# Kernel tuning notes

Hardware: AMD Instinct MI355X
Metric: run time of the kernel (lower is better)

The kernel has to match this reference:

```python
import jax, jax.numpy as jnp
import numpy as np
from jax import lax


def _gather_xq(x_flat, qx, qy, w):
    # x_flat: [B, C, H*W]; qx, qy: [B, H, W] int32 -> [B, C, H, W]
    b, c, _ = x_flat.shape
    h, ww = qx.shape[1], qx.shape[2]
    idx = (qx * w + qy).reshape(b, 1, h * ww)  # [B,1,H*W]
    out = jnp.take_along_axis(x_flat, jnp.broadcast_to(idx, (b, c, h * ww)), axis=2)
    return out.reshape(b, c, h, ww)


def setup_inputs() -> dict:
    key = jax.random.key(0)
    k1, k2 = jax.random.split(key)
    B, C, H, W = 8, 256, 128, 128
    x = jax.random.normal(k1, (B, C, H, W), dtype=jnp.float32)
    w_conv = jax.random.normal(k2, (2, C, 3, 3), dtype=jnp.float32) * 0.02
    b_conv = jnp.zeros((2,), dtype=jnp.float32)
    return {"x": x, "w_conv": w_conv, "b_conv": b_conv}


def reference(x, w_conv, b_conv):
    B, C, H, W = x.shape
    # offset conv: Conv2d(inc, 2, k=3, stride=1, padding=1)
    offset = lax.conv_general_dilated(
        x, w_conv, window_strides=(1, 1), padding=((1, 1), (1, 1)),
        dimension_numbers=("NCHW", "OIHW", "NCHW"),
    ) + b_conv[None, :, None, None]  # [B, 2, H, W], N = 1

    # base grid p_0 (ij indexing as in torch.meshgrid legacy)
    p0_x = jnp.arange(H, dtype=x.dtype)[:, None] * jnp.ones((1, W), dtype=x.dtype)
    p0_y = jnp.ones((H, 1), dtype=x.dtype) * jnp.arange(W, dtype=x.dtype)[None, :]
    px = p0_x[None] + offset[:, 0]  # [B, H, W]
    py = p0_y[None] + offset[:, 1]

    px = jnp.clip(px, 0.0, H - 2)
    py = jnp.clip(py, 0.0, W - 2)

    # corner indices (detached in original via requires_grad=False)
    fx = lax.stop_gradient(jnp.floor(px))
    fy = lax.stop_gradient(jnp.floor(py))
    qx0 = fx.astype(jnp.int32)
    qy0 = fy.astype(jnp.int32)
    qx1 = qx0 + 1
    qy1 = qy0 + 1

    # bilinear weights
    g_lt = (1.0 + (fx - px)) * (1.0 + (fy - py))
    g_rb = (1.0 - (fx + 1.0 - px)) * (1.0 - (fy + 1.0 - py))
    g_lb = (1.0 + (fx - px)) * (1.0 - (fy + 1.0 - py))
    g_rt = (1.0 - (fx + 1.0 - px)) * (1.0 + (fy - py))

    x_flat = x.reshape(B, C, H * W)
    x_lt = _gather_xq(x_flat, qx0, qy0, W)
    x_rb = _gather_xq(x_flat, qx1, qy1, W)
    x_lb = _gather_xq(x_flat, qx0, qy1, W)
    x_rt = _gather_xq(x_flat, qx1, qy0, W)

    out = (g_lt[:, None] * x_lt + g_rb[:, None] * x_rb
           + g_lb[:, None] * x_lb + g_rt[:, None] * x_rt)  # [B, C, H, W]
    # original returns x_up_reset.squeeze(1): with C>1 and N=1 this keeps
    # the trailing sampling-point dim -> [B, C, H, W, 1]
    return out[..., None]
```

## Files before the change

kernel.cpp:

```cpp
#include <hip/hip_runtime.h>

#define Bn 8
#define Cn 256
#define Hn 128
#define Wn 128
#define NPIX (Bn * Hn * Wn)

#define CCH 4
#define CPC (Cn / CCH)

__global__ __launch_bounds__(256, 8) void conv_partial_kernel(
    const float* __restrict__ x, const float* __restrict__ wconv,
    float2* __restrict__ part)
{
    const int pg    = blockIdx.x & 511;
    const int chunk = blockIdx.x >> 9;
    const int gid = pg * 256 + threadIdx.x;
    const int w = gid & (Wn - 1);
    const int h = (gid >> 7) & (Hn - 1);
    const int b = gid >> 14;

    const float* xb = x + ((size_t)b * Cn + chunk * CPC) * (Hn * Wn) + h * Wn + w;

    const bool hm = (h > 0), hp = (h < Hn - 1);
    const bool wm = (w > 0), wp = (w < Wn - 1);

    float acc0 = 0.f, acc1 = 0.f;
    const float* w0b = wconv + chunk * CPC * 9;
    const float* w1b = wconv + Cn * 9 + chunk * CPC * 9;

    #pragma unroll 2
    for (int c = 0; c < CPC; ++c) {
        const float* xc = xb + c * (Hn * Wn);
        float v00 = (hm && wm) ? xc[-Wn - 1] : 0.f;
        float v01 = (hm)       ? xc[-Wn]     : 0.f;
        float v02 = (hm && wp) ? xc[-Wn + 1] : 0.f;
        float v10 = (wm)       ? xc[-1]      : 0.f;
        float v11 =              xc[0];
        float v12 = (wp)       ? xc[1]       : 0.f;
        float v20 = (hp && wm) ? xc[Wn - 1]  : 0.f;
        float v21 = (hp)       ? xc[Wn]      : 0.f;
        float v22 = (hp && wp) ? xc[Wn + 1]  : 0.f;

        const float* w0 = w0b + c * 9;
        const float* w1 = w1b + c * 9;
        acc0 = fmaf(v00, w0[0], acc0); acc0 = fmaf(v01, w0[1], acc0);
        acc0 = fmaf(v02, w0[2], acc0); acc0 = fmaf(v10, w0[3], acc0);
        acc0 = fmaf(v11, w0[4], acc0); acc0 = fmaf(v12, w0[5], acc0);
        acc0 = fmaf(v20, w0[6], acc0); acc0 = fmaf(v21, w0[7], acc0);
        acc0 = fmaf(v22, w0[8], acc0);
        acc1 = fmaf(v00, w1[0], acc1); acc1 = fmaf(v01, w1[1], acc1);
        acc1 = fmaf(v02, w1[2], acc1); acc1 = fmaf(v10, w1[3], acc1);
        acc1 = fmaf(v11, w1[4], acc1); acc1 = fmaf(v12, w1[5], acc1);
        acc1 = fmaf(v20, w1[6], acc1); acc1 = fmaf(v21, w1[7], acc1);
        acc1 = fmaf(v22, w1[8], acc1);
    }

    part[(size_t)chunk * NPIX + gid] = make_float2(acc0, acc1);
}

#define SCH 8
#define SPC (Cn / SCH)

__global__ __launch_bounds__(256, 8) void sample_kernel(
    const float* __restrict__ x, const float2* __restrict__ part,
    const float* __restrict__ bconv, float* __restrict__ out)
{
    const int tid = blockIdx.x * 256 + threadIdx.x;
    const int hw = tid & (Hn * Wn - 1);
    const int r  = tid >> 14;
    const int chunk = r & (SCH - 1);
    const int b = r >> 3;
    const int gid = (b << 14) | hw;
    const int w = hw & (Wn - 1);
    const int h = hw >> 7;

    float2 p0 = part[gid];
    float2 p1 = part[NPIX + gid];
    float2 p2 = part[2 * NPIX + gid];
    float2 p3 = part[3 * NPIX + gid];
    float off0 = p0.x + p1.x + p2.x + p3.x + bconv[0];
    float off1 = p0.y + p1.y + p2.y + p3.y + bconv[1];

    float px = (float)h + off0;
    float py = (float)w + off1;
    px = fminf(fmaxf(px, 0.f), (float)(Hn - 2));
    py = fminf(fmaxf(py, 0.f), (float)(Wn - 2));
    float fx = floorf(px), fy = floorf(py);
    float dx = px - fx, dy = py - fy;
    int bs = (int)fx * Wn + (int)fy;

    float glt = (1.f - dx) * (1.f - dy);
    float grb = dx * dy;
    float glb = (1.f - dx) * dy;
    float grt = dx * (1.f - dy);

    const float* xb = x + ((size_t)b * Cn + chunk * SPC) * (Hn * Wn) + bs;
    float* ob = out + ((size_t)b * Cn + chunk * SPC) * (Hn * Wn) + hw;

    #pragma unroll 8
    for (int c = 0; c < SPC; ++c) {
        const float* xc = xb + c * (Hn * Wn);
        float lt = xc[0];
        float lb = xc[1];
        float rt = xc[Wn];
        float rb = xc[Wn + 1];
        float v = glt * lt + grb * rb + glb * lb + grt * rt;
        __builtin_nontemporal_store(v, ob + c * (Hn * Wn));
    }
}

extern "C" void kernel_launch(void* const* d_in, const int* in_sizes, int n_in,
                              void* d_out, int out_size, void* d_ws, size_t ws_size,
                              hipStream_t stream) {
    const float* x     = (const float*)d_in[0];
    const float* wconv = (const float*)d_in[1];
    const float* bconv = (const float*)d_in[2];
    float* out = (float*)d_out;

    float2* part = (float2*)d_ws;

    conv_partial_kernel<<<(NPIX / 256) * CCH, 256, 0, stream>>>(x, wconv, part);
    sample_kernel<<<(NPIX * SCH) / 256, 256, 0, stream>>>(x, part, bconv, out);
}
```

Baseline: 337.2 us.

## Compute four conv outputs per thread and two sample pixels per thread

The offset conv now has each thread produce four adjacent output columns. It loads each input row as a float4 plus two halo values, so neighbouring taps are reused from registers. The sampling kernel handles two horizontally adjacent pixels per thread, using paired float2 gathers for the bilinear corners and vectorized nontemporal stores. This aims to cut redundant global loads and instruction overhead, at the cost of more registers, lower occupancy bounds and fewer threads in flight.

```diff
diff --git a/kernel.cpp b/kernel.cpp
--- a/kernel.cpp
+++ b/kernel.cpp
@@ -4,59 +4,78 @@
 #define Cn 256
 #define Hn 128
 #define Wn 128
+#define HW (Hn * Wn)
 #define NPIX (Bn * Hn * Wn)
+
+typedef float v2f  __attribute__((ext_vector_type(2)));
+typedef float v2fu __attribute__((ext_vector_type(2), aligned(4)));
+typedef float v4f  __attribute__((ext_vector_type(4)));
 
 #define CCH 4
 #define CPC (Cn / CCH)
 
-__global__ __launch_bounds__(256, 8) void conv_partial_kernel(
+__global__ __launch_bounds__(256, 4) void conv_partial_kernel(
     const float* __restrict__ x, const float* __restrict__ wconv,
     float2* __restrict__ part)
 {
-    const int pg    = blockIdx.x & 511;
-    const int chunk = blockIdx.x >> 9;
-    const int gid = pg * 256 + threadIdx.x;
-    const int w = gid & (Wn - 1);
-    const int h = (gid >> 7) & (Hn - 1);
-    const int b = gid >> 14;
+    const int pg    = blockIdx.x & 127;
+    const int chunk = blockIdx.x >> 7;
+    const int pq = pg * 256 + (int)threadIdx.x;
+    const int w0 = (pq & 31) << 2;
+    const int h  = (pq >> 5) & (Hn - 1);
+    const int b  = pq >> 12;
 
-    const float* xb = x + ((size_t)b * Cn + chunk * CPC) * (Hn * Wn) + h * Wn + w;
+    const float* xb = x + ((size_t)(b * Cn + chunk * CPC)) * HW + h * Wn + w0;
 
     const bool hm = (h > 0), hp = (h < Hn - 1);
-    const bool wm = (w > 0), wp = (w < Wn - 1);
+    const bool wm = (w0 > 0), wp = (w0 < Wn - 4);
 
-    float acc0 = 0.f, acc1 = 0.f;
+    float a00 = 0.f, a01 = 0.f, a02 = 0.f, a03 = 0.f;
+    float a10 = 0.f, a11 = 0.f, a12 = 0.f, a13 = 0.f;
+
     const float* w0b = wconv + chunk * CPC * 9;
     const float* w1b = wconv + Cn * 9 + chunk * CPC * 9;
 
     #pragma unroll 2
     for (int c = 0; c < CPC; ++c) {
-        const float* xc = xb + c * (Hn * Wn);
-        float v00 = (hm && wm) ? xc[-Wn - 1] : 0.f;
-        float v01 = (hm)       ? xc[-Wn]     : 0.f;
-        float v02 = (hm && wp) ? xc[-Wn + 1] : 0.f;
-        float v10 = (wm)       ? xc[-1]      : 0.f;
-        float v11 =              xc[0];
-        float v12 = (wp)       ? xc[1]       : 0.f;
-        float v20 = (hp && wm) ? xc[Wn - 1]  : 0.f;
-        float v21 = (hp)       ? xc[Wn]      : 0.f;
-        float v22 = (hp && wp) ? xc[Wn + 1]  : 0.f;
-
-        const float* w0 = w0b + c * 9;
-        const float* w1 = w1b + c * 9;
-        acc0 = fmaf(v00, w0[0], acc0); acc0 = fmaf(v01, w0[1], acc0);
-        acc0 = fmaf(v02, w0[2], acc0); acc0 = fmaf(v10, w0[3], acc0);
-        acc0 = fmaf(v11, w0[4], acc0); acc0 = fmaf(v12, w0[5], acc0);
-        acc0 = fmaf(v20, w0[6], acc0); acc0 = fmaf(v21, w0[7], acc0);
-        acc0 = fmaf(v22, w0[8], acc0);
-        acc1 = fmaf(v00, w1[0], acc1); acc1 = fmaf(v01, w1[1], acc1);
-        acc1 = fmaf(v02, w1[2], acc1); acc1 = fmaf(v10, w1[3], acc1);
-        acc1 = fmaf(v11, w1[4], acc1); acc1 = fmaf(v12, w1[5], acc1);
-        acc1 = fmaf(v20, w1[6], acc1); acc1 = fmaf(v21, w1[7], acc1);
-        acc1 = fmaf(v22, w1[8], acc1);
+        const float* xc = xb + c * HW;
+        float v[3][6];
+        #pragma unroll
+        for (int r = 0; r < 3; ++r) {
+            const float* rp = xc + (r - 1) * Wn;
+            const bool vld = (r == 0) ? hm : (r == 2) ? hp : true;
+            if (vld) {
+                const float4 m = *(const float4*)rp;
+                v[r][0] = wm ? rp[-1] : 0.f;
+                v[r][1] = m.x; v[r][2] = m.y; v[r][3] = m.z; v[r][4] = m.w;
+                v[r][5] = wp ? rp[4] : 0.f;
+            } else {
+                v[r][0] = 0.f; v[r][1] = 0.f; v[r][2] = 0.f;
+                v[r][3] = 0.f; v[r][4] = 0.f; v[r][5] = 0.f;
+            }
+        }
+        const float* w0c = w0b + c * 9;
+        const float* w1c = w1b + c * 9;
+        #pragma unroll
+        for (int r = 0; r < 3; ++r) {
+            const float k0 = w0c[r*3+0], k1 = w0c[r*3+1], k2 = w0c[r*3+2];
+            const float u0 = w1c[r*3+0], u1 = w1c[r*3+1], u2 = w1c[r*3+2];
+            a00 = fmaf(v[r][0], k0, a00); a00 = fmaf(v[r][1], k1, a00); a00 = fmaf(v[r][2], k2, a00);
+            a01 = fmaf(v[r][1], k0, a01); a01 = fmaf(v[r][2], k1, a01); a01 = fmaf(v[r][3], k2, a01);
+            a02 = fmaf(v[r][2], k0, a02); a02 = fmaf(v[r][3], k1, a02); a02 = fmaf(v[r][4], k2, a02);
+            a03 = fmaf(v[r][3], k0, a03); a03 = fmaf(v[r][4], k1, a03); a03 = fmaf(v[r][5], k2, a03);
+            a10 = fmaf(v[r][0], u0, a10); a10 = fmaf(v[r][1], u1, a10); a10 = fmaf(v[r][2], u2, a10);
+            a11 = fmaf(v[r][1], u0, a11); a11 = fmaf(v[r][2], u1, a11); a11 = fmaf(v[r][3], u2, a11);
+            a12 = fmaf(v[r][2], u0, a12); a12 = fmaf(v[r][3], u1, a12); a12 = fmaf(v[r][4], u2, a12);
+            a13 = fmaf(v[r][3], u0, a13); a13 = fmaf(v[r][4], u1, a13); a13 = fmaf(v[r][5], u2, a13);
+        }
     }
 
-    part[(size_t)chunk * NPIX + gid] = make_float2(acc0, acc1);
+    v4f* pt = (v4f*)(part + (size_t)chunk * NPIX + ((size_t)pq << 2));
+    v4f s0 = {a00, a10, a01, a11};
+    v4f s1 = {a02, a12, a03, a13};
+    pt[0] = s0;
+    pt[1] = s1;
 }
 
 #define SCH 8
@@ -66,47 +85,54 @@
     const float* __restrict__ x, const float2* __restrict__ part,
     const float* __restrict__ bconv, float* __restrict__ out)
 {
-    const int tid = blockIdx.x * 256 + threadIdx.x;
-    const int hw = tid & (Hn * Wn - 1);
-    const int r  = tid >> 14;
-    const int chunk = r & (SCH - 1);
-    const int b = r >> 3;
-    const int gid = (b << 14) | hw;
-    const int w = hw & (Wn - 1);
-    const int h = hw >> 7;
+    const int tid = blockIdx.x * 256 + (int)threadIdx.x;
+    const int pp    = tid & (NPIX / 2 - 1);
+    const int chunk = tid >> 16;
+    const int pr  = pp & (HW / 2 - 1);
+    const int b   = pp >> 13;
+    const int hw0 = pr << 1;
+    const int w = hw0 & (Wn - 1);
+    const int h = hw0 >> 7;
 
-    float2 p0 = part[gid];
-    float2 p1 = part[NPIX + gid];
-    float2 p2 = part[2 * NPIX + gid];
-    float2 p3 = part[3 * NPIX + gid];
-    float off0 = p0.x + p1.x + p2.x + p3.x + bconv[0];
-    float off1 = p0.y + p1.y + p2.y + p3.y + bconv[1];
+    const v4f* p4 = (const v4f*)part;
+    v4f q = p4[pp] + p4[(NPIX / 2) + pp] + p4[2 * (NPIX / 2) + pp] + p4[3 * (NPIX / 2) + pp];
 
-    float px = (float)h + off0;
-    float py = (float)w + off1;
-    px = fminf(fmaxf(px, 0.f), (float)(Hn - 2));
-    py = fminf(fmaxf(py, 0.f), (float)(Wn - 2));
-    float fx = floorf(px), fy = floorf(py);
-    float dx = px - fx, dy = py - fy;
-    int bs = (int)fx * Wn + (int)fy;
+    const float bc0 = bconv[0], bc1 = bconv[1];
+    float px0 = (float)h + q.x + bc0;
+    float py0 = (float)w + q.y + bc1;
+    float px1 = (float)h + q.z + bc0;
+    float py1 = (float)(w + 1) + q.w + bc1;
+    px0 = fminf(fmaxf(px0, 0.f), (float)(Hn - 2));
+    py0 = fminf(fmaxf(py0, 0.f), (float)(Wn - 2));
+    px1 = fminf(fmaxf(px1, 0.f), (float)(Hn - 2));
+    py1 = fminf(fmaxf(py1, 0.f), (float)(Wn - 2));
+    const float fx0 = floorf(px0), fy0 = floorf(py0);
+    const float fx1 = floorf(px1), fy1 = floorf(py1);
+    const float dx0 = px0 - fx0, dy0 = py0 - fy0;
+    const float dx1 = px1 - fx1, dy1 = py1 - fy1;
+    const int bs0 = (int)fx0 * Wn + (int)fy0;
+    const int bs1 = (int)fx1 * Wn + (int)fy1;
 
-    float glt = (1.f - dx) * (1.f - dy);
-    float grb = dx * dy;
-    float glb = (1.f - dx) * dy;
-    float grt = dx * (1.f - dy);
+    const float glt0 = (1.f - dx0) * (1.f - dy0), grb0 = dx0 * dy0;
+    const float glb0 = (1.f - dx0) * dy0,         grt0 = dx0 * (1.f - dy0);
+    const float glt1 = (1.f - dx1) * (1.f - dy1), grb1 = dx1 * dy1;
+    const float glb1 = (1.f - dx1) * dy1,         grt1 = dx1 * (1.f - dy1);
 
-    const float* xb = x + ((size_t)b * Cn + chunk * SPC) * (Hn * Wn) + bs;
-    float* ob = out + ((size_t)b * Cn + chunk * SPC) * (Hn * Wn) + hw;
+    const size_t cb = ((size_t)(b * Cn + chunk * SPC)) * HW;
+    const float* xb = x + cb;
+    float* ob = out + cb + hw0;
 
-    #pragma unroll 8
+    #pragma unroll 4
     for (int c = 0; c < SPC; ++c) {
-        const float* xc = xb + c * (Hn * Wn);
-        float lt = xc[0];
-        float lb = xc[1];
-        float rt = xc[Wn];
-        float rb = xc[Wn + 1];
-        float v = glt * lt + grb * rb + glb * lb + grt * rt;
-        __builtin_nontemporal_store(v, ob + c * (Hn * Wn));
+        const float* xc = xb + (size_t)c * HW;
+        v2fu A0 = *(const v2fu*)(xc + bs0);
+        v2fu B0 = *(const v2fu*)(xc + bs0 + Wn);
+        v2fu A1 = *(const v2fu*)(xc + bs1);
+        v2fu B1 = *(const v2fu*)(xc + bs1 + Wn);
+        const float o0 = glt0 * A0.x + glb0 * A0.y + grt0 * B0.x + grb0 * B0.y;
+        const float o1 = glt1 * A1.x + glb1 * A1.y + grt1 * B1.x + grb1 * B1.y;
+        v2f o = {o0, o1};
+        __builtin_nontemporal_store(o, (v2f*)(ob + (size_t)c * HW));
     }
 }
 
@@ -120,6 +146,6 @@
 
     float2* part = (float2*)d_ws;
 
-    conv_partial_kernel<<<(NPIX / 256) * CCH, 256, 0, stream>>>(x, wconv, part);
-    sample_kernel<<<(NPIX * SCH) / 256, 256, 0, stream>>>(x, part, bconv, out);
+    conv_partial_kernel<<<(NPIX / 4 / 256) * CCH, 256, 0, stream>>>(x, wconv, part);
+    sample_kernel<<<(NPIX / 2 * SCH) / 256, 256, 0, stream>>>(x, part, bconv, out);
 }
```

New measurement: 337.6 us. No clear change (+0.1%).
